# Performance work log

Hardware: AMD Instinct MI355X
Metric: run time of the kernel (lower is better)

The kernel has to match this reference:

```python
import jax, jax.numpy as jnp
import numpy as np

D_MODEL = 1024
N_HEADS = 16
HEAD_DIM = D_MODEL // N_HEADS
ROPE_BASE = 10000.0


def setup_inputs() -> dict:
    key = jax.random.key(0)
    ks = jax.random.split(key, 5)
    B, S = 1, 4096
    scale = 1.0 / np.sqrt(D_MODEL)
    x = jax.random.normal(ks[0], (B, S, D_MODEL), dtype=jnp.float32)
    Wq = jax.random.normal(ks[1], (D_MODEL, D_MODEL), dtype=jnp.float32) * scale
    Wk = jax.random.normal(ks[2], (D_MODEL, D_MODEL), dtype=jnp.float32) * scale
    Wv = jax.random.normal(ks[3], (D_MODEL, D_MODEL), dtype=jnp.float32) * scale
    Wo = jax.random.normal(ks[4], (D_MODEL, D_MODEL), dtype=jnp.float32) * scale
    return {"x": x, "Wq": Wq, "Wk": Wk, "Wv": Wv, "Wo": Wo}


def _rope(q, k):
    # q, k: [B, S, H, Dh]
    S, Dh = q.shape[1], q.shape[-1]
    inv_freq = 1.0 / (ROPE_BASE ** (jnp.arange(0, Dh, 2, dtype=jnp.float32) / Dh))
    t = jnp.arange(S, dtype=jnp.float32)
    freqs = jnp.outer(t, inv_freq)                      # [S, Dh/2]
    emb = jnp.concatenate([freqs, freqs], axis=-1)      # [S, Dh]
    cos = jnp.cos(emb)[None, :, None, :]                # [1, S, 1, Dh]
    sin = jnp.sin(emb)[None, :, None, :]

    def rotate_half(v):
        v1, v2 = v[..., : Dh // 2], v[..., Dh // 2 :]
        return jnp.concatenate([-v2, v1], axis=-1)

    return q * cos + rotate_half(q) * sin, k * cos + rotate_half(k) * sin


def reference(x, Wq, Wk, Wv, Wo):
    B, S, _ = x.shape
    H, Dh = N_HEADS, HEAD_DIM
    # torch Linear: y = x @ W.T
    q = (x @ Wq.T).reshape(B, S, H, Dh)
    k = (x @ Wk.T).reshape(B, S, H, Dh)
    v = (x @ Wv.T).reshape(B, S, H, Dh)
    q, k = _rope(q, k)
    scale = 1.0 / np.sqrt(Dh)
    # scores: [B, H, S, S]
    scores = jnp.einsum("bqhd,bkhd->bhqk", q, k) * scale
    causal = jnp.triu(jnp.ones((S, S), dtype=bool), k=1)
    scores = jnp.where(causal, -jnp.inf, scores)
    attn = jax.nn.softmax(scores, axis=-1)
    out = jnp.einsum("bhqk,bkhd->bqhd", attn, v).reshape(B, S, H * Dh)
    return out @ Wo.T
```

## Files before the change

### kernel.cpp

```cpp
#include <hip/hip_runtime.h>
#include <hip/hip_bf16.h>

typedef __attribute__((ext_vector_type(8))) short bf16x8;
typedef __attribute__((ext_vector_type(4))) float f32x4;
typedef unsigned short u16;

#define S_LEN 4096
#define DM 1024
#define NH 16
#define DH 64
#define PSTR 72

__device__ __forceinline__ u16 f2b_rne(float f) {
  unsigned u = __builtin_bit_cast(unsigned, f);
  return (u16)((u + 0x7fffu + ((u >> 16) & 1u)) >> 16);
}
__device__ __forceinline__ unsigned pk2(float a, float b) {
  unsigned ua = __builtin_bit_cast(unsigned, a);
  unsigned ub = __builtin_bit_cast(unsigned, b);
  ua = (ua + 0x7fffu + ((ua >> 16) & 1u)) >> 16;
  ub = (ub + 0x7fffu + ((ub >> 16) & 1u)) & 0xffff0000u;
  return ua | ub;
}
__device__ __forceinline__ unsigned pk2t(float a, float b) {
  return __builtin_amdgcn_perm(__builtin_bit_cast(unsigned, b),
                               __builtin_bit_cast(unsigned, a), 0x07060302u);
}

__device__ __forceinline__ void glds16(const u16* g, u16* l) {
  __builtin_amdgcn_global_load_lds(
      (const __attribute__((address_space(1))) unsigned int*)g,
      (__attribute__((address_space(3))) unsigned int*)l, 16, 0, 0);
}

__global__ __launch_bounds__(256) void cvt_all(const float* __restrict__ x,
                                               const float* __restrict__ Wq,
                                               const float* __restrict__ Wk,
                                               const float* __restrict__ Wv,
                                               const float* __restrict__ Wo,
                                               u16* __restrict__ xb, u16* __restrict__ wqb,
                                               u16* __restrict__ wkb, u16* __restrict__ wvb,
                                               u16* __restrict__ wob) {
  int idx = (blockIdx.x * 256 + threadIdx.x) * 4;
  const float* src;
  u16* dst;
  int o;
  if (idx < 4194304) {
    src = x; dst = xb; o = idx;
  } else {
    int t = idx - 4194304;
    int wsel = t >> 20;
    o = t & 1048575;
    src = (wsel == 0) ? Wq : (wsel == 1) ? Wk : (wsel == 2) ? Wv : Wo;
    dst = (wsel == 0) ? wqb : (wsel == 1) ? wkb : (wsel == 2) ? wvb : wob;
  }
  float4 v = *(const float4*)(src + o);
  uint2 ov;
  ov.x = pk2(v.x, v.y);
  ov.y = pk2(v.z, v.w);
  *(uint2*)(dst + o) = ov;
}

__global__ __launch_bounds__(256) void zero_kernel(float4* __restrict__ p) {
  p[blockIdx.x * 256 + threadIdx.x] = float4{0.f, 0.f, 0.f, 0.f};
}

__global__ __launch_bounds__(256) void qkv_gemm(const u16* __restrict__ A,
                                                const u16* __restrict__ Wq,
                                                const u16* __restrict__ Wk,
                                                const u16* __restrict__ Wv,
                                                u16* __restrict__ Qo, u16* __restrict__ Ko,
                                                u16* __restrict__ Vt) {
  __shared__ __align__(16) u16 As[2 * 128 * 32];
  __shared__ __align__(16) u16 Bs[2 * 128 * 32];
  const int mat = blockIdx.x >> 3;
  const u16* B = (mat == 0) ? Wq : (mat == 1) ? Wk : Wv;
  const int K = DM, N = DM;
  const int tid = threadIdx.x;
  const int wave = tid >> 6, lane = tid & 63;
  const int fm = lane & 15, fq = lane >> 4;
  const int mb = blockIdx.y * 128, nb = (blockIdx.x & 7) * 128;
  const int wm = (wave & 1) * 64, wn = (wave >> 1) * 64;

  f32x4 acc[4][4];
#pragma unroll
  for (int i = 0; i < 4; ++i)
#pragma unroll
    for (int j = 0; j < 4; ++j)
#pragma unroll
      for (int r = 0; r < 4; ++r) acc[i][j][r] = 0.f;

  const int r_ = tid >> 2;
  const int cg = (tid & 3) ^ ((r_ >> 1) & 3);
  const u16* Ag0 = A + (size_t)(mb + r_) * K + cg * 8;
  const u16* Ag1 = A + (size_t)(mb + r_ + 64) * K + cg * 8;
  const u16* Bg0 = B + (size_t)(nb + r_) * K + cg * 8;
  const u16* Bg1 = B + (size_t)(nb + r_ + 64) * K + cg * 8;
  const int l0 = wave * 512;
  const int l1 = 2048 + wave * 512;
  const int sw = (fm >> 1) & 3;

  int buf = 0;
  glds16(Ag0, As + l0);
  glds16(Ag1, As + l1);
  glds16(Bg0, Bs + l0);
  glds16(Bg1, Bs + l1);

  for (int k0 = 0; k0 < K; k0 += 32) {
    __syncthreads();
    if (k0 + 32 < K) {
      int bo = (buf ^ 1) * 4096;
      glds16(Ag0 + k0 + 32, As + bo + l0);
      glds16(Ag1 + k0 + 32, As + bo + l1);
      glds16(Bg0 + k0 + 32, Bs + bo + l0);
      glds16(Bg1 + k0 + 32, Bs + bo + l1);
    }
    const u16* Ab = As + buf * 4096;
    const u16* Bb = Bs + buf * 4096;
    bf16x8 av[4], bv[4];
#pragma unroll
    for (int t = 0; t < 4; ++t) {
      av[t] = *(const bf16x8*)(Ab + (wm + t * 16 + fm) * 32 + ((fq ^ sw) * 8));
      bv[t] = *(const bf16x8*)(Bb + (wn + t * 16 + fm) * 32 + ((fq ^ sw) * 8));
    }
#pragma unroll
    for (int i = 0; i < 4; ++i)
#pragma unroll
      for (int j = 0; j < 4; ++j)
        acc[i][j] = __builtin_amdgcn_mfma_f32_16x16x32_bf16(av[i], bv[j], acc[i][j], 0, 0, 0);
    buf ^= 1;
  }

  if (mat < 2) {
    u16* Out = (mat == 0) ? Qo : Ko;
    const float qs = (mat == 0) ? 0.1803368801111204f : 1.0f;
    const float c1 = -9.2103403719761836f / 32.f;
    const float if0 = __expf((float)fm * c1);
    const float if1 = __expf((float)(16 + fm) * c1);
#pragma unroll
    for (int ii = 0; ii < 4; ++ii) {
#pragma unroll
      for (int r = 0; r < 4; ++r) {
        float s = (float)(mb + wm + ii * 16 + fq * 4 + r);
#pragma unroll
        for (int jp = 0; jp < 2; ++jp) {
          float ang = s * (jp ? if1 : if0);
          float sn, cs;
          __sincosf(ang, &sn, &cs);
          float a = acc[ii][jp][r], b = acc[ii][jp + 2][r];
          acc[ii][jp][r] = (a * cs - b * sn) * qs;
          acc[ii][jp + 2][r] = (b * cs + a * sn) * qs;
        }
      }
    }
#pragma unroll
    for (int i = 0; i < 4; ++i)
#pragma unroll
      for (int j = 0; j < 4; ++j)
#pragma unroll
        for (int r = 0; r < 4; ++r) {
          int row = mb + wm + i * 16 + fq * 4 + r;
          int col = nb + wn + j * 16 + fm;
          Out[(size_t)row * N + col] = f2b_rne(acc[i][j][r]);
        }
  } else {
#pragma unroll
    for (int i = 0; i < 4; ++i)
#pragma unroll
      for (int j = 0; j < 4; ++j) {
        int col = nb + wn + j * 16 + fm;
        int row0 = mb + wm + i * 16 + fq * 4;
        uint2 pv;
        pv.x = pk2(acc[i][j][0], acc[i][j][1]);
        pv.y = pk2(acc[i][j][2], acc[i][j][3]);
        *(uint2*)(Vt + (size_t)col * S_LEN + row0) = pv;
      }
  }
}

__global__ __launch_bounds__(256) void o_gemm(const u16* __restrict__ A,
                                              const u16* __restrict__ B,
                                              float* __restrict__ C, int M, int N, int K) {
  __shared__ __align__(16) u16 As[2 * 64 * 32];
  __shared__ __align__(16) u16 Bs[2 * 128 * 32];
  const int tid = threadIdx.x;
  const int wave = tid >> 6, lane = tid & 63;
  const int fm = lane & 15, fq = lane >> 4;
  const int mb = blockIdx.y * 64, nb = blockIdx.x * 128;
  const int wm = (wave & 1) * 32, wn = (wave >> 1) * 64;

  f32x4 acc[2][4];
#pragma unroll
  for (int i = 0; i < 2; ++i)
#pragma unroll
    for (int j = 0; j < 4; ++j)
#pragma unroll
      for (int r = 0; r < 4; ++r) acc[i][j][r] = 0.f;

  const int r_ = tid >> 2;
  const int cg = (tid & 3) ^ ((r_ >> 1) & 3);
  const u16* Ag0 = A + (size_t)(mb + r_) * K + cg * 8;
  const u16* Bg0 = B + (size_t)(nb + r_) * K + cg * 8;
  const u16* Bg1 = B + (size_t)(nb + r_ + 64) * K + cg * 8;
  const int l0 = wave * 512;
  const int l1 = 2048 + wave * 512;
  const int sw = (fm >> 1) & 3;

  int buf = 0;
  glds16(Ag0, As + l0);
  glds16(Bg0, Bs + l0);
  glds16(Bg1, Bs + l1);

  for (int k0 = 0; k0 < K; k0 += 32) {
    __syncthreads();
    if (k0 + 32 < K) {
      int aoff = (buf ^ 1) * 2048, boff = (buf ^ 1) * 4096;
      glds16(Ag0 + k0 + 32, As + aoff + l0);
      glds16(Bg0 + k0 + 32, Bs + boff + l0);
      glds16(Bg1 + k0 + 32, Bs + boff + l1);
    }
    const u16* Ab = As + buf * 2048;
    const u16* Bb = Bs + buf * 4096;
    bf16x8 av[2], bv[4];
#pragma unroll
    for (int t = 0; t < 2; ++t)
      av[t] = *(const bf16x8*)(Ab + (wm + t * 16 + fm) * 32 + ((fq ^ sw) * 8));
#pragma unroll
    for (int t = 0; t < 4; ++t)
      bv[t] = *(const bf16x8*)(Bb + (wn + t * 16 + fm) * 32 + ((fq ^ sw) * 8));
#pragma unroll
    for (int i = 0; i < 2; ++i)
#pragma unroll
      for (int j = 0; j < 4; ++j)
        acc[i][j] = __builtin_amdgcn_mfma_f32_16x16x32_bf16(av[i], bv[j], acc[i][j], 0, 0, 0);
    buf ^= 1;
  }
#pragma unroll
  for (int i = 0; i < 2; ++i)
#pragma unroll
    for (int j = 0; j < 4; ++j)
#pragma unroll
      for (int r = 0; r < 4; ++r) {
        int row = mb + wm + i * 16 + fq * 4 + r;
        int col = nb + wn + j * 16 + fm;
        C[(size_t)row * N + col] = acc[i][j][r];
      }
}

__global__ __launch_bounds__(512, 4) void attn_kernel(const u16* __restrict__ Q,
                                                      const u16* __restrict__ K,
                                                      const u16* __restrict__ Vt,
                                                      float* __restrict__ Oacc,
                                                      float* __restrict__ Lacc) {
  __shared__ __align__(16) u16 Ks[2 * 4096];
  __shared__ __align__(16) u16 Vs[2 * 4096];
  __shared__ __align__(16) u16 Ps[8][16 * PSTR];
  const int tid = threadIdx.x;
  const int w = tid >> 6, lane = tid & 63;
  const int fm = lane & 15, fq = lane >> 4;
  const int bid = blockIdx.x;
  const int u = bid & 255, hi = bid >> 8;
  const int h = u & 15;
  const int qt0 = u >> 4;
  const int qt = hi ? qt0 : 15 - qt0;
  const int half = hi;
  const int qb = qt * 256 + w * 32;
  const int nlocal = 2 * qt + 2;
  const int kbase = half * nlocal;
  const int dtile = qb >> 6;

  bf16x8 q0[2], q1[2];
#pragma unroll
  for (int g = 0; g < 2; ++g) {
    const u16* qp = Q + (size_t)(qb + g * 16 + fm) * DM + h * DH + fq * 8;
    q0[g] = *(const bf16x8*)(qp);
    q1[g] = *(const bf16x8*)(qp + 32);
  }
  f32x4 o[2][4];
  f32x4 ls[2];
#pragma unroll
  for (int g = 0; g < 2; ++g) {
#pragma unroll
    for (int r = 0; r < 4; ++r) ls[g][r] = 0.f;
#pragma unroll
    for (int c4 = 0; c4 < 4; ++c4)
#pragma unroll
      for (int r = 0; r < 4; ++r) o[g][c4][r] = 0.f;
  }
  const short ONEB = (short)0x3F80;
  const bf16x8 vone = {ONEB, ONEB, ONEB, ONEB, ONEB, ONEB, ONEB, ONEB};

  const int rr = tid >> 3;
  const int cc8 = (tid & 7) ^ (rr & 7);
  const u16* Kg = K + (size_t)rr * DM + h * DH + cc8 * 8;
  const u16* Vg = Vt + (size_t)(h * DH + rr) * S_LEN + cc8 * 8;
  const int l0 = w * 512;
  const int sw7 = fm & 7;
  const f32x4 zf = {0.f, 0.f, 0.f, 0.f};

  glds16(Kg + (size_t)kbase * 64 * DM, Ks + l0);
  glds16(Vg + kbase * 64, Vs + l0);

  int buf = 0;
  for (int kl = 0; kl < nlocal; ++kl) {
    const int ktg = kbase + kl;
    __syncthreads();
    if (kl + 1 < nlocal) {
      int bo = (buf ^ 1) * 4096;
      glds16(Kg + (size_t)(ktg + 1) * 64 * DM, Ks + bo + l0);
      glds16(Vg + (ktg + 1) * 64, Vs + bo + l0);
    }
    if (ktg <= dtile) {
      const u16* Kb = Ks + buf * 4096;
      const u16* Vb = Vs + buf * 4096;

      f32x4 st[2][4];
#pragma unroll
      for (int t = 0; t < 4; ++t) {
        const u16* kr = Kb + (t * 16 + fm) * 64;
        bf16x8 ka = *(const bf16x8*)(kr + ((fq ^ sw7) * 8));
        bf16x8 kb2 = *(const bf16x8*)(kr + (((fq + 4) ^ sw7) * 8));
#pragma unroll
        for (int g = 0; g < 2; ++g) {
          f32x4 s = __builtin_amdgcn_mfma_f32_16x16x32_bf16(ka, q0[g], zf, 0, 0, 0);
          st[g][t] = __builtin_amdgcn_mfma_f32_16x16x32_bf16(kb2, q1[g], s, 0, 0, 0);
        }
      }
      if (ktg == dtile) {
#pragma unroll
        for (int g = 0; g < 2; ++g) {
          int qg = qb + g * 16 + fm;
#pragma unroll
          for (int t = 0; t < 4; ++t) {
            int key = ktg * 64 + t * 16 + fq * 4;
#pragma unroll
            for (int r = 0; r < 4; ++r)
              st[g][t][r] = (key + r > qg) ? -1e30f : st[g][t][r];
          }
        }
      }
      bf16x8 pvb[4][2];
#pragma unroll
      for (int c4 = 0; c4 < 4; ++c4) {
        const u16* vr = Vb + (c4 * 16 + fm) * 64;
        pvb[c4][0] = *(const bf16x8*)(vr + ((fq ^ sw7) * 8));
        pvb[c4][1] = *(const bf16x8*)(vr + (((fq + 4) ^ sw7) * 8));
      }
#pragma unroll
      for (int g = 0; g < 2; ++g) {
#pragma unroll
        for (int t = 0; t < 4; ++t) {
          float p0 = __builtin_amdgcn_exp2f(st[g][t][0]);
          float p1 = __builtin_amdgcn_exp2f(st[g][t][1]);
          float p2 = __builtin_amdgcn_exp2f(st[g][t][2]);
          float p3 = __builtin_amdgcn_exp2f(st[g][t][3]);
          uint2 pk;
          pk.x = pk2t(p0, p1);
          pk.y = pk2t(p2, p3);
          *(uint2*)(&Ps[w][fm * PSTR + t * 16 + fq * 4]) = pk;
        }
        asm volatile("s_waitcnt lgkmcnt(0)" ::: "memory");
        bf16x8 ap0 = *(const bf16x8*)(&Ps[w][fm * PSTR + fq * 8]);
        bf16x8 ap1 = *(const bf16x8*)(&Ps[w][fm * PSTR + 32 + fq * 8]);
        ls[g] = __builtin_amdgcn_mfma_f32_16x16x32_bf16(ap0, vone, ls[g], 0, 0, 0);
        ls[g] = __builtin_amdgcn_mfma_f32_16x16x32_bf16(ap1, vone, ls[g], 0, 0, 0);
#pragma unroll
        for (int c4 = 0; c4 < 4; ++c4) {
          o[g][c4] = __builtin_amdgcn_mfma_f32_16x16x32_bf16(ap0, pvb[c4][0], o[g][c4], 0, 0, 0);
          o[g][c4] = __builtin_amdgcn_mfma_f32_16x16x32_bf16(ap1, pvb[c4][1], o[g][c4], 0, 0, 0);
        }
      }
    }
    buf ^= 1;
  }
  float* Ob = Oacc + ((size_t)h * S_LEN + qt * 256 + w * 32) * DH;
  float* Lb = Lacc + h * S_LEN + qt * 256 + w * 32;
#pragma unroll
  for (int g = 0; g < 2; ++g) {
    if (fm == 0) {
#pragma unroll
      for (int r = 0; r < 4; ++r)
        unsafeAtomicAdd(Lb + g * 16 + fq * 4 + r, ls[g][r]);
    }
#pragma unroll
    for (int c4 = 0; c4 < 4; ++c4)
#pragma unroll
      for (int r = 0; r < 4; ++r)
        unsafeAtomicAdd(Ob + (g * 16 + fq * 4 + r) * DH + c4 * 16 + fm, o[g][c4][r]);
  }
}

__global__ __launch_bounds__(256) void combine_kernel(const float* __restrict__ Oacc,
                                                      const float* __restrict__ Lacc,
                                                      u16* __restrict__ Ctx) {
  int idx = blockIdx.x * 256 + threadIdx.x;
  int d4 = (idx & 15) * 4;
  int hh = (idx >> 4) & 15;
  int row = idx >> 8;
  float4 a = *(const float4*)(Oacc + ((size_t)hh * S_LEN + row) * DH + d4);
  float il = 1.0f / Lacc[hh * S_LEN + row];
  uint2 o;
  o.x = pk2(a.x * il, a.y * il);
  o.y = pk2(a.z * il, a.w * il);
  *(uint2*)(Ctx + (size_t)row * DM + hh * DH + d4) = o;
}

extern "C" void kernel_launch(void* const* d_in, const int* in_sizes, int n_in,
                              void* d_out, int out_size, void* d_ws, size_t ws_size,
                              hipStream_t stream) {
  const float* x  = (const float*)d_in[0];
  const float* Wq = (const float*)d_in[1];
  const float* Wk = (const float*)d_in[2];
  const float* Wv = (const float*)d_in[3];
  const float* Wo = (const float*)d_in[4];
  float* out = (float*)d_out;

  const size_t MB = 1u << 20;
  char* ws = (char*)d_ws;
  u16* xb    = (u16*)(ws + 0 * MB);
  u16* wqb   = (u16*)(ws + 8 * MB);
  u16* wkb   = (u16*)(ws + 10 * MB);
  u16* wvb   = (u16*)(ws + 12 * MB);
  float* Oacc = (float*)(ws + 0 * MB);
  float* Lacc = (float*)(ws + 16 * MB);
  u16* wob   = (u16*)(ws + 17 * MB);
  u16* Qb    = (u16*)(ws + 19 * MB);
  u16* Kb    = (u16*)(ws + 27 * MB);
  u16* Vtb   = (u16*)(ws + 35 * MB);
  u16* Ctx   = (u16*)(ws + 43 * MB);

  cvt_all<<<8192, 256, 0, stream>>>(x, Wq, Wk, Wv, Wo, xb, wqb, wkb, wvb, wob);
  qkv_gemm<<<dim3(24, 32), 256, 0, stream>>>(xb, wqb, wkb, wvb, Qb, Kb, Vtb);
  zero_kernel<<<4160, 256, 0, stream>>>((float4*)Oacc);
  attn_kernel<<<512, 512, 0, stream>>>(Qb, Kb, Vtb, Oacc, Lacc);
  combine_kernel<<<4096, 256, 0, stream>>>(Oacc, Lacc, Ctx);
  o_gemm<<<dim3(8, 64), 256, 0, stream>>>(Ctx, wob, out, S_LEN, DM, DM);
}
```

Before: 229.7 us.

## Fuse softmax normalization into output GEMM and split attention keys four ways

The combine kernel is removed. The output-projection GEMM now reads the float attention accumulators directly, scales each row by the inverse softmax sum, converts to bf16 and stores the result into shared memory itself. The attention grid doubles to 1024 blocks, splitting each query tile's key range into quarters instead of halves, with a new block-to-tile ordering. This is meant to cut a kernel launch and an intermediate bf16 round trip and to improve load balance, at the cost of more atomic traffic and A-operand loads that are no longer asynchronous.

```diff
diff --git a/kernel.cpp b/kernel.cpp
--- a/kernel.cpp
+++ b/kernel.cpp
@@ -178,9 +178,10 @@
   }
 }
 
-__global__ __launch_bounds__(256) void o_gemm(const u16* __restrict__ A,
+__global__ __launch_bounds__(256) void o_gemm(const float* __restrict__ Oacc,
+                                              const float* __restrict__ Lacc,
                                               const u16* __restrict__ B,
-                                              float* __restrict__ C, int M, int N, int K) {
+                                              float* __restrict__ C) {
   __shared__ __align__(16) u16 As[2 * 64 * 32];
   __shared__ __align__(16) u16 Bs[2 * 128 * 32];
   const int tid = threadIdx.x;
@@ -199,25 +200,42 @@
 
   const int r_ = tid >> 2;
   const int cg = (tid & 3) ^ ((r_ >> 1) & 3);
-  const u16* Ag0 = A + (size_t)(mb + r_) * K + cg * 8;
-  const u16* Bg0 = B + (size_t)(nb + r_) * K + cg * 8;
-  const u16* Bg1 = B + (size_t)(nb + r_ + 64) * K + cg * 8;
+  const int arow = mb + r_;
+  float il[16];
+#pragma unroll
+  for (int hh = 0; hh < 16; ++hh) il[hh] = 1.0f / Lacc[hh * S_LEN + arow];
+
+  const u16* Bg0 = B + (size_t)(nb + r_) * DM + cg * 8;
+  const u16* Bg1 = B + (size_t)(nb + r_ + 64) * DM + cg * 8;
   const int l0 = wave * 512;
   const int l1 = 2048 + wave * 512;
   const int sw = (fm >> 1) & 3;
+  const int awr = r_ * 32 + (tid & 3) * 8;
 
   int buf = 0;
-  glds16(Ag0, As + l0);
   glds16(Bg0, Bs + l0);
   glds16(Bg1, Bs + l1);
-
-  for (int k0 = 0; k0 < K; k0 += 32) {
+  float4 a0 = *(const float4*)(Oacc + (size_t)arow * 64 + cg * 8);
+  float4 a1 = *(const float4*)(Oacc + (size_t)arow * 64 + cg * 8 + 4);
+
+#pragma unroll
+  for (int k0 = 0; k0 < DM; k0 += 32) {
+    const float ih = il[k0 >> 6];
+    uint4 aw;
+    aw.x = pk2(a0.x * ih, a0.y * ih);
+    aw.y = pk2(a0.z * ih, a0.w * ih);
+    aw.z = pk2(a1.x * ih, a1.y * ih);
+    aw.w = pk2(a1.z * ih, a1.w * ih);
+    *(uint4*)(As + buf * 2048 + awr) = aw;
     __syncthreads();
-    if (k0 + 32 < K) {
-      int aoff = (buf ^ 1) * 2048, boff = (buf ^ 1) * 4096;
-      glds16(Ag0 + k0 + 32, As + aoff + l0);
-      glds16(Bg0 + k0 + 32, Bs + boff + l0);
-      glds16(Bg1 + k0 + 32, Bs + boff + l1);
+    if (k0 + 32 < DM) {
+      int bo = (buf ^ 1) * 4096;
+      glds16(Bg0 + k0 + 32, Bs + bo + l0);
+      glds16(Bg1 + k0 + 32, Bs + bo + l1);
+      const float* ap = Oacc + ((size_t)((k0 + 32) >> 6) * S_LEN + arow) * 64 +
+                        ((k0 + 32) & 63) + cg * 8;
+      a0 = *(const float4*)(ap);
+      a1 = *(const float4*)(ap + 4);
     }
     const u16* Ab = As + buf * 2048;
     const u16* Bb = Bs + buf * 4096;
@@ -243,7 +261,7 @@
       for (int r = 0; r < 4; ++r) {
         int row = mb + wm + i * 16 + fq * 4 + r;
         int col = nb + wn + j * 16 + fm;
-        C[(size_t)row * N + col] = acc[i][j][r];
+        C[(size_t)row * DM + col] = acc[i][j][r];
       }
 }
 
@@ -259,14 +277,14 @@
   const int w = tid >> 6, lane = tid & 63;
   const int fm = lane & 15, fq = lane >> 4;
   const int bid = blockIdx.x;
-  const int u = bid & 255, hi = bid >> 8;
-  const int h = u & 15;
-  const int qt0 = u >> 4;
-  const int qt = hi ? qt0 : 15 - qt0;
-  const int half = hi;
+  const int p = bid >> 3, hl = bid & 7;
+  const int r4 = p >> 5, jj = (p >> 3) & 3;
+  const int quarter = (p >> 1) & 3, hh = p & 1;
+  const int qt = 15 - (4 * r4 + ((jj + r4) & 3));
+  const int h = hh * 8 + hl;
   const int qb = qt * 256 + w * 32;
-  const int nlocal = 2 * qt + 2;
-  const int kbase = half * nlocal;
+  const int nlocal = qt + 1;
+  const int kbase = quarter * nlocal;
   const int dtile = qb >> 6;
 
   bf16x8 q0[2], q1[2];
@@ -388,21 +406,6 @@
       for (int r = 0; r < 4; ++r)
         unsafeAtomicAdd(Ob + (g * 16 + fq * 4 + r) * DH + c4 * 16 + fm, o[g][c4][r]);
   }
-}
-
-__global__ __launch_bounds__(256) void combine_kernel(const float* __restrict__ Oacc,
-                                                      const float* __restrict__ Lacc,
-                                                      u16* __restrict__ Ctx) {
-  int idx = blockIdx.x * 256 + threadIdx.x;
-  int d4 = (idx & 15) * 4;
-  int hh = (idx >> 4) & 15;
-  int row = idx >> 8;
-  float4 a = *(const float4*)(Oacc + ((size_t)hh * S_LEN + row) * DH + d4);
-  float il = 1.0f / Lacc[hh * S_LEN + row];
-  uint2 o;
-  o.x = pk2(a.x * il, a.y * il);
-  o.y = pk2(a.z * il, a.w * il);
-  *(uint2*)(Ctx + (size_t)row * DM + hh * DH + d4) = o;
 }
 
 extern "C" void kernel_launch(void* const* d_in, const int* in_sizes, int n_in,
@@ -427,12 +430,10 @@
   u16* Qb    = (u16*)(ws + 19 * MB);
   u16* Kb    = (u16*)(ws + 27 * MB);
   u16* Vtb   = (u16*)(ws + 35 * MB);
-  u16* Ctx   = (u16*)(ws + 43 * MB);
 
   cvt_all<<<8192, 256, 0, stream>>>(x, Wq, Wk, Wv, Wo, xb, wqb, wkb, wvb, wob);
   qkv_gemm<<<dim3(24, 32), 256, 0, stream>>>(xb, wqb, wkb, wvb, Qb, Kb, Vtb);
   zero_kernel<<<4160, 256, 0, stream>>>((float4*)Oacc);
-  attn_kernel<<<512, 512, 0, stream>>>(Qb, Kb, Vtb, Oacc, Lacc);
-  combine_kernel<<<4096, 256, 0, stream>>>(Oacc, Lacc, Ctx);
-  o_gemm<<<dim3(8, 64), 256, 0, stream>>>(Ctx, wob, out, S_LEN, DM, DM);
-}
+  attn_kernel<<<1024, 512, 0, stream>>>(Qb, Kb, Vtb, Oacc, Lacc);
+  o_gemm<<<dim3(8, 64), 256, 0, stream>>>(Oacc, Lacc, wob, out);
+}
```

Result: slower. 256.6 us (+11.7%).
